# Performance work log

Measured on AMD Instinct MI355X. Metric: run time of the kernel, lower is better.

The kernel has to match this reference:

```python
import jax, jax.numpy as jnp
import numpy as np

L, NK = 4, 6  # num blocks, Nk geodesic components

def _gelu(x):
    return jax.nn.gelu(x, approximate=False)  # torch nn.GELU default (erf)

def _ln(x, g, b, eps=1e-5):
    m = jnp.mean(x, axis=-1, keepdims=True)
    v = jnp.mean((x - m) ** 2, axis=-1, keepdims=True)
    return (x - m) * jax.lax.rsqrt(v + eps) * g + b


def setup_inputs() -> dict:
    B, N, C, M = 4, 8192, 64, 64
    key = jax.random.key(0)
    ks = iter(jax.random.split(key, 48))
    def nrm(*s):
        return jax.random.normal(next(ks), s, dtype=jnp.float32) * 0.02
    inp = {
        'x': jax.random.normal(next(ks), (B, N, 1), dtype=jnp.float32),
        'MATRIX_Phy': jax.random.normal(next(ks), (N, M), dtype=jnp.float32) * 0.02,
        'INVERSE_Phy': jax.random.normal(next(ks), (M, N), dtype=jnp.float32) * 0.02,
        'meshPoints': jax.random.normal(next(ks), (N, 3), dtype=jnp.float32),
        'adj_norm': jax.random.uniform(next(ks), (N, N), dtype=jnp.float32) / N,
    }
    inp.update(
        fc0_w=nrm(4, C), fc0_b=jnp.zeros(C), fc01_w=nrm(C, C), fc01_b=jnp.zeros(C),
        blk_ln1_g=jnp.ones((L, C)), blk_ln1_b=jnp.zeros((L, C)),
        norm1_g=jnp.ones((L, C)), norm1_b=jnp.zeros((L, C)),
        spec_w=jax.random.uniform(next(ks), (L, NK, C, C, M), dtype=jnp.float32) / (C * C),
        enc_p1_w=nrm(L, 3, C), enc_p1_b=jnp.zeros((L, C)),
        enc_p2_w=nrm(L, C, C), enc_p2_b=jnp.zeros((L, C)),
        enc_g1_w=nrm(L, C, C), enc_g1_b=jnp.zeros((L, C)),
        enc_g2_w=nrm(L, C, C), enc_g2_b=jnp.zeros((L, C)),
        enc_o1_w=nrm(L, C, 2 * C), enc_o1_b=jnp.zeros((L, 2 * C)),
        enc_o2_w=nrm(L, 2 * C, NK), enc_o2_b=jnp.zeros((L, NK)),
        spat_g1_w=nrm(L, C, 2 * C), spat_g1_b=jnp.zeros((L, 2 * C)),
        spat_g2_w=nrm(L, 2 * C, C), spat_g2_b=jnp.zeros((L, C)),
        blk_ln2_g=jnp.ones((L, C)), blk_ln2_b=jnp.zeros((L, C)),
        mlp_pre_w=nrm(L, C, 2 * C), mlp_pre_b=jnp.zeros((L, 2 * C)),
        mlp_post_w=nrm(L, 2 * C, C), mlp_post_b=jnp.zeros((L, C)),
        ln1_g=jnp.ones(C), ln1_b=jnp.zeros(C),
        fc1_w=nrm(C, 128), fc1_b=jnp.zeros(128),
        fc2_w=nrm(128, 1), fc2_b=jnp.zeros(1),
    )
    return inp


def reference(x, MATRIX_Phy, INVERSE_Phy, meshPoints, adj_norm,
              fc0_w, fc0_b, fc01_w, fc01_b,
              blk_ln1_g, blk_ln1_b, norm1_g, norm1_b, spec_w,
              enc_p1_w, enc_p1_b, enc_p2_w, enc_p2_b,
              enc_g1_w, enc_g1_b, enc_g2_w, enc_g2_b,
              enc_o1_w, enc_o1_b, enc_o2_w, enc_o2_b,
              spat_g1_w, spat_g1_b, spat_g2_w, spat_g2_b,
              blk_ln2_g, blk_ln2_b, mlp_pre_w, mlp_pre_b, mlp_post_w, mlp_post_b,
              ln1_g, ln1_b, fc1_w, fc1_b, fc2_w, fc2_b):
    B = x.shape[0]
    mesh = jnp.broadcast_to(meshPoints[None], (B,) + meshPoints.shape)  # [B,N,3]
    h = jnp.concatenate([x, mesh], axis=-1)                             # [B,N,4]
    h = h @ fc0_w + fc0_b
    h = h @ fc01_w + fc01_b                                             # [B,N,C]
    for l in range(L):
        z = _ln(h, blk_ln1_g[l], blk_ln1_b[l])
        # --- MeshGCN encoder -> geodesic mixing coefficients geoT [M,Nk] ---
        e = _gelu(meshPoints @ enc_p1_w[l] + enc_p1_b[l]) @ enc_p2_w[l] + enc_p2_b[l]
        e = _gelu(adj_norm @ (e @ enc_g1_w[l] + enc_g1_b[l]))
        e = adj_norm @ (e @ enc_g2_w[l] + enc_g2_b[l])
        e = (e @ enc_o1_w[l] + enc_o1_b[l]) @ enc_o2_w[l] + enc_o2_b[l]  # [N,Nk]
        geoT = jax.nn.softmax(INVERSE_Phy @ e, axis=1)                   # [M,Nk]
        # --- geodesic-modulated spectral conv ---
        cm = jnp.einsum('mn,bnc->bcm', INVERSE_Phy, z)                   # [B,C,M]
        w = jnp.einsum('kiom,mk->iom', spec_w[l], geoT)                  # [C,C,M]
        cg = jnp.einsum('bim,iom->bom', cm, w)                           # [B,C,M]
        x1 = jnp.einsum('bom,nm->bno', cg, MATRIX_Phy)                   # [B,N,C]
        x1 = _ln(x1, norm1_g[l], norm1_b[l])
        # --- spatial GCN branch (SimpleGCN: gcn->relu->gcn) ---
        s = jax.nn.relu(jnp.einsum('mn,bnc->bmc', adj_norm, z @ spat_g1_w[l] + spat_g1_b[l]))
        x2 = jnp.einsum('mn,bnc->bmc', adj_norm, s @ spat_g2_w[l] + spat_g2_b[l])
        h = x1 + x2 + h
        z2 = _ln(h, blk_ln2_g[l], blk_ln2_b[l])
        h = _gelu(z2 @ mlp_pre_w[l] + mlp_pre_b[l]) @ mlp_post_w[l] + mlp_post_b[l] + h
    h = _gelu(_ln(h, ln1_g, ln1_b) @ fc1_w + fc1_b)
    return h @ fc2_w + fc2_b                                             # [B,N,1]
```

## Files before the change

kernel.cpp:

```cpp
#include <hip/hip_runtime.h>
#include <math.h>

typedef __bf16 bf16_t;
typedef __bf16 bf16x8 __attribute__((ext_vector_type(8)));
typedef __bf16 bf16x4 __attribute__((ext_vector_type(4)));
typedef float  f32x4  __attribute__((ext_vector_type(4)));

#define NN 8192
#define RA 8320
#define GPS256 2129920u
#define GPS512 4259840u
#define XPAD 68
#define X2PAD 132
#define ZTPAD 66

__device__ __forceinline__ float gelu_f(float x) {
    return 0.5f * x * (1.0f + erff(x * 0.70710678118654752f));
}

__device__ __forceinline__ float wsum64(float v) {
#pragma unroll
    for (int m = 32; m; m >>= 1) v += __shfl_xor(v, m);
    return v;
}

__device__ __forceinline__ float gp4(const float* __restrict__ Gp, size_t gi) {
    return (Gp[gi] + Gp[gi + (size_t)GPS256]) + (Gp[gi + 2 * (size_t)GPS256] + Gp[gi + 3 * (size_t)GPS256]);
}

__device__ __forceinline__ float gpn(const float* __restrict__ Gp, size_t gi, size_t st, int ns) {
    float v = Gp[gi];
    for (int s = 1; s < ns; ++s) v += Gp[gi + (size_t)s * st];
    return v;
}

__device__ __forceinline__ void async16(const void* g, void* l) {
    __builtin_amdgcn_global_load_lds(
        (const __attribute__((address_space(1))) unsigned int*)g,
        (__attribute__((address_space(3))) unsigned int*)l,
        16, 0, 0);
}

__device__ __forceinline__ void mm16(const float* __restrict__ X, int xpad,
                                     const float* __restrict__ W, int ws, int K,
                                     int c, int r0, float* acc) {
    for (int k0 = 0; k0 < K; k0 += 4) {
        float w0 = W[(size_t)(k0 + 0) * ws + c];
        float w1 = W[(size_t)(k0 + 1) * ws + c];
        float w2 = W[(size_t)(k0 + 2) * ws + c];
        float w3 = W[(size_t)(k0 + 3) * ws + c];
#pragma unroll
        for (int i = 0; i < 16; ++i) {
            float4 xv = *(const float4*)(X + (size_t)(r0 + i) * xpad + k0);
            acc[i] = fmaf(xv.x, w0, acc[i]);
            acc[i] = fmaf(xv.y, w1, acc[i]);
            acc[i] = fmaf(xv.z, w2, acc[i]);
            acc[i] = fmaf(xv.w, w3, acc[i]);
        }
    }
}

__global__ __launch_bounds__(256) void k_adj_convert(const float* __restrict__ adj,
                                                     const float* __restrict__ INV,
                                                     bf16_t* __restrict__ adjB,
                                                     float* __restrict__ rowsum) {
    int row = blockIdx.x;
    int t = threadIdx.x;
    bf16_t* br = adjB + (size_t)row * NN;
    if (row >= NN + 64) {
        bf16x4 zz; zz[0] = zz[1] = zz[2] = zz[3] = (bf16_t)0.f;
#pragma unroll
        for (int v = 0; v < 8; ++v) *(bf16x4*)(br + (v * 256 + t) * 4) = zz;
        return;
    }
    const float* ar = (row < NN) ? adj + (size_t)row * NN : INV + (size_t)(row - NN) * NN;
    float s = 0.f;
#pragma unroll
    for (int v = 0; v < 8; ++v) {
        int i = (v * 256 + t) * 4;
        float4 f = *(const float4*)(ar + i);
        s += f.x + f.y + f.z + f.w;
        bf16x4 o;
        o[0] = (bf16_t)f.x; o[1] = (bf16_t)f.y; o[2] = (bf16_t)f.z; o[3] = (bf16_t)f.w;
        *(bf16x4*)(br + i) = o;
    }
    if (row < NN) {
        s = wsum64(s);
        __shared__ float w4[4];
        if ((t & 63) == 0) w4[t >> 6] = s;
        __syncthreads();
        if (t == 0) rowsum[row] = w4[0] + w4[1] + w4[2] + w4[3];
    }
}

__global__ __launch_bounds__(64) void k_fold(const float* __restrict__ fc0w, const float* __restrict__ fc0b,
                                             const float* __restrict__ fc01w, const float* __restrict__ fc01b,
                                             float* __restrict__ W0b) {
    int c = threadIdx.x;
#pragma unroll
    for (int j = 0; j < 4; ++j) {
        float a = 0.f;
        for (int k = 0; k < 64; ++k) a += fc0w[j * 64 + k] * fc01w[k * 64 + c];
        W0b[j * 64 + c] = a;
    }
    float b = fc01b[c];
    for (int k = 0; k < 64; ++k) b += fc0b[k] * fc01w[k * 64 + c];
    W0b[256 + c] = b;
}

__global__ __launch_bounds__(256) void k_init_h(const float* __restrict__ x, const float* __restrict__ mesh,
                         const float* __restrict__ W0b,
                         const float* __restrict__ zg, const float* __restrict__ zb,
                         float* __restrict__ h, bf16_t* __restrict__ Vt) {
    __shared__ __align__(16) char buf[64 * ZTPAD * 2];
    bf16_t* ZT = (bf16_t*)buf;
    int t = threadIdx.x, c = t & 63, rq = t >> 6, r0 = rq * 16;
    int bb = blockIdx.x >> 7, n0 = (blockIdx.x & 127) * 64;
    float w0c = W0b[c], w1c = W0b[64 + c], w2c = W0b[128 + c], w3c = W0b[192 + c], b0c = W0b[256 + c];
    float gc = zg[c], bc = zb[c];
#pragma unroll
    for (int q = 0; q < 16; ++q) {
        int n = n0 + r0 + q;
        int w = bb * NN + n;
        float xv = x[w];
        float m0 = mesh[n * 3], m1 = mesh[n * 3 + 1], m2 = mesh[n * 3 + 2];
        float hv = b0c + xv * w0c + m0 * w1c + m1 * w2c + m2 * w3c;
        h[(size_t)w * 64 + c] = hv;
        float s = wsum64(hv), s2 = wsum64(hv * hv);
        float mean = s * (1.f / 64.f), var = s2 * (1.f / 64.f) - mean * mean;
        float z = (hv - mean) * rsqrtf(var + 1e-5f) * gc + bc;
        ZT[c * ZTPAD + r0 + q] = (bf16_t)z;
    }
    __syncthreads();
#pragma unroll
    for (int cc = 0; cc < 16; ++cc) {
        int c2 = r0 + cc;
        Vt[(size_t)(256 + bb * 64 + c2) * NN + n0 + c] = ZT[c2 * ZTPAD + c];
    }
}

__global__ __launch_bounds__(256) void k_enc_pre(const float* __restrict__ mesh,
                          const float* __restrict__ p1w, const float* __restrict__ p1b,
                          const float* __restrict__ p2w, const float* __restrict__ p2b,
                          const float* __restrict__ g1w, const float* __restrict__ g1b,
                          bf16_t* __restrict__ Vt) {
    __shared__ __align__(16) char buf[2 * 64 * XPAD * 4];
    float* X1 = (float*)buf;
    float* X2 = (float*)(buf + 64 * XPAD * 4);
    bf16_t* ZT = (bf16_t*)buf;
    int t = threadIdx.x, c = t & 63, rq = t >> 6, r0 = rq * 16;
    int ll = blockIdx.x >> 7, n0 = (blockIdx.x & 127) * 64;
    float p1b_c = p1b[ll * 64 + c];
    float p1w0 = p1w[(ll * 3 + 0) * 64 + c], p1w1 = p1w[(ll * 3 + 1) * 64 + c], p1w2 = p1w[(ll * 3 + 2) * 64 + c];
#pragma unroll
    for (int q = 0; q < 16; ++q) {
        int n = n0 + r0 + q;
        float m0 = mesh[n * 3], m1 = mesh[n * 3 + 1], m2 = mesh[n * 3 + 2];
        X1[(r0 + q) * XPAD + c] = gelu_f(p1b_c + m0 * p1w0 + m1 * p1w1 + m2 * p1w2);
    }
    __syncthreads();
    float e2[16];
#pragma unroll
    for (int i = 0; i < 16; ++i) e2[i] = p2b[ll * 64 + c];
    mm16(X1, XPAD, p2w + ll * 4096, 64, 64, c, r0, e2);
    __syncthreads();
#pragma unroll
    for (int q = 0; q < 16; ++q) X2[(r0 + q) * XPAD + c] = e2[q];
    __syncthreads();
    float tt[16];
#pragma unroll
    for (int i = 0; i < 16; ++i) tt[i] = g1b[ll * 64 + c];
    mm16(X2, XPAD, g1w + ll * 4096, 64, 64, c, r0, tt);
#pragma unroll
    for (int q = 0; q < 16; ++q) ZT[c * ZTPAD + r0 + q] = (bf16_t)tt[q];
    __syncthreads();
#pragma unroll
    for (int cc = 0; cc < 16; ++cc) {
        int c2 = r0 + cc;
        Vt[(size_t)(ll * 64 + c2) * NN + n0 + c] = ZT[c2 * ZTPAD + c];
    }
}

__global__ __launch_bounds__(256) void k_enc_mid(const float* __restrict__ Gp,
                          const float* __restrict__ g2w, const float* __restrict__ g2b,
                          bf16_t* __restrict__ Vt) {
    __shared__ __align__(16) char buf[64 * XPAD * 4 + 64 * ZTPAD * 2];
    float* X = (float*)buf;
    bf16_t* ZT = (bf16_t*)(buf + 64 * XPAD * 4);
    int t = threadIdx.x, c = t & 63, rq = t >> 6, r0 = rq * 16;
    int ll = blockIdx.x >> 7, n0 = (blockIdx.x & 127) * 64;
#pragma unroll
    for (int q = 0; q < 16; ++q) {
        int n = n0 + r0 + q;
        X[(r0 + q) * XPAD + c] = gelu_f(gp4(Gp, (size_t)n * 256 + ll * 64 + c));
    }
    __syncthreads();
    float t2[16];
#pragma unroll
    for (int i = 0; i < 16; ++i) t2[i] = g2b[ll * 64 + c];
    mm16(X, XPAD, g2w + ll * 4096, 64, 64, c, r0, t2);
#pragma unroll
    for (int q = 0; q < 16; ++q) ZT[c * ZTPAD + r0 + q] = (bf16_t)t2[q];
    __syncthreads();
#pragma unroll
    for (int cc = 0; cc < 16; ++cc) {
        int c2 = r0 + cc;
        Vt[(size_t)(ll * 64 + c2) * NN + n0 + c] = ZT[c2 * ZTPAD + c];
    }
}

__global__ void k_geo_part(const float* __restrict__ Gp,
                           const float* __restrict__ o1w, const float* __restrict__ o1b,
                           const float* __restrict__ o2w, const float* __restrict__ o2b,
                           const float* __restrict__ INV,
                           float* __restrict__ partials) {
    int l = blockIdx.x >> 7, chunk = blockIdx.x & 127;
    int n0 = chunk * 64;
    int t = threadIdx.x;
    __shared__ float e4L[64][65];
    for (int r = 0; r < 64; ++r) {
        size_t gi = (size_t)(n0 + r) * 512 + l * 64 + t;
        e4L[r][t] = Gp[gi] + Gp[gi + (size_t)GPS512];
    }
    __syncthreads();
    float X[64];
#pragma unroll
    for (int i = 0; i < 64; ++i) X[i] = e4L[t][i];
    float e5[6] = {0, 0, 0, 0, 0, 0};
    const float* o1wl = o1w + (size_t)l * 64 * 128;
    const float* o2wl = o2w + (size_t)l * 128 * 6;
    for (int j = 0; j < 128; ++j) {
        float a = o1b[l * 128 + j];
#pragma unroll
        for (int i = 0; i < 64; ++i) a += X[i] * o1wl[i * 128 + j];
#pragma unroll
        for (int k = 0; k < 6; ++k) e5[k] += a * o2wl[j * 6 + k];
    }
#pragma unroll
    for (int k = 0; k < 6; ++k) e5[k] += o2b[l * 6 + k];
    __shared__ float e5L[64][8];
#pragma unroll
    for (int k = 0; k < 6; ++k) e5L[t][k] = e5[k];
    __syncthreads();
    float p[6] = {0, 0, 0, 0, 0, 0};
    const float* ivr = INV + (size_t)t * NN + n0;
    for (int r = 0; r < 64; ++r) {
        float iv = ivr[r];
#pragma unroll
        for (int k = 0; k < 6; ++k) p[k] += iv * e5L[r][k];
    }
#pragma unroll
    for (int k = 0; k < 6; ++k) partials[(size_t)(((l * 128 + chunk) * 64) + t) * 6 + k] = p[k];
}

__global__ void k_geo_final(const float* __restrict__ partials, float* __restrict__ geoT) {
    int l = blockIdx.x, m = threadIdx.x;
    float g[6] = {0, 0, 0, 0, 0, 0};
    for (int ch = 0; ch < 128; ++ch) {
#pragma unroll
        for (int k = 0; k < 6; ++k) g[k] += partials[(size_t)(((l * 128 + ch) * 64) + m) * 6 + k];
    }
    float mx = g[0];
#pragma unroll
    for (int k = 1; k < 6; ++k) mx = fmaxf(mx, g[k]);
    float s = 0.f;
#pragma unroll
    for (int k = 0; k < 6; ++k) { g[k] = expf(g[k] - mx); s += g[k]; }
    float inv = 1.f / s;
#pragma unroll
    for (int k = 0; k < 6; ++k) geoT[(size_t)(l * 64 + m) * 6 + k] = g[k] * inv;
}

__global__ __launch_bounds__(64) void k_w(const float* __restrict__ specw,
                                          const float* __restrict__ geoT,
                                          float* __restrict__ wAll) {
    int l = blockIdx.x >> 12, io = blockIdx.x & 4095;
    int m = threadIdx.x;
    float a = 0.f;
#pragma unroll
    for (int k = 0; k < 6; ++k)
        a += specw[(((size_t)l * 6 + k) * 4096 + io) * 64 + m] * geoT[(size_t)(l * 64 + m) * 6 + k];
    wAll[((size_t)l * 4096 + io) * 64 + m] = a;
}

__global__ __launch_bounds__(256) void k_cmsum(const float* __restrict__ Gp, float* __restrict__ cmc,
                                               int ncols, int colbase, int ns) {
    int bi = blockIdx.x * 4 + (threadIdx.x >> 6);
    int m = threadIdx.x & 63;
    size_t st = (size_t)RA * ncols;
    size_t gi = (size_t)(NN + m) * ncols + colbase + bi;
    cmc[bi * 64 + m] = gpn(Gp, gi, st, ns);
}

__global__ __launch_bounds__(256) void k_cg2(const float* __restrict__ cmc,
                                             const float* __restrict__ wl,
                                             float* __restrict__ cgT) {
    int o = blockIdx.x;
    int b = threadIdx.x >> 6, m = threadIdx.x & 63;
    float acc = 0.f;
    for (int i = 0; i < 64; ++i)
        acc += cmc[(b * 64 + i) * 64 + m] * wl[((size_t)(i * 64 + o)) * 64 + m];
    cgT[(b * 64 + m) * 64 + o] = acc;
}

__global__ __launch_bounds__(256) void k_spat_mid(const float* __restrict__ Gp,
                           const float* __restrict__ W1, const float* __restrict__ b1,
                           const float* __restrict__ W2, const float* __restrict__ b2,
                           const float* __restrict__ rowsum, bf16_t* __restrict__ Vt,
                           int ncols, int colbase, int ns) {
    __shared__ __align__(16) char buf[64 * XPAD * 4 + 64 * X2PAD * 4];
    float* X  = (float*)buf;
    float* X2 = (float*)(buf + 64 * XPAD * 4);
    bf16_t* ZT = (bf16_t*)buf;
    int t = threadIdx.x, c = t & 63, rq = t >> 6, r0 = rq * 16;
    int bb = blockIdx.x >> 7, n0 = (blockIdx.x & 127) * 64;
    size_t st = (size_t)RA * ncols;
    float rs[16];
#pragma unroll
    for (int q = 0; q < 16; ++q) {
        int m = n0 + r0 + q;
        rs[q] = rowsum[m];
        X[(r0 + q) * XPAD + c] = gpn(Gp, (size_t)m * ncols + colbase + bb * 64 + c, st, ns);
    }
    __syncthreads();
    float ma0[16], ma1[16];
    float b1c0 = b1[c], b1c1 = b1[64 + c];
#pragma unroll
    for (int i = 0; i < 16; ++i) { ma0[i] = rs[i] * b1c0; ma1[i] = rs[i] * b1c1; }
    mm16(X, XPAD, W1, 128, 64, c, r0, ma0);
    mm16(X, XPAD, W1 + 64, 128, 64, c, r0, ma1);
    __syncthreads();
#pragma unroll
    for (int q = 0; q < 16; ++q) {
        X2[(r0 + q) * X2PAD + c] = fmaxf(ma0[q], 0.f);
        X2[(r0 + q) * X2PAD + 64 + c] = fmaxf(ma1[q], 0.f);
    }
    __syncthreads();
    float y[16];
#pragma unroll
    for (int i = 0; i < 16; ++i) y[i] = b2[c];
    mm16(X2, X2PAD, W2, 64, 128, c, r0, y);
#pragma unroll
    for (int q = 0; q < 16; ++q) ZT[c * ZTPAD + r0 + q] = (bf16_t)y[q];
    __syncthreads();
#pragma unroll
    for (int cc = 0; cc < 16; ++cc) {
        int c2 = r0 + cc;
        Vt[(size_t)(bb * 64 + c2) * NN + n0 + c] = ZT[c2 * ZTPAD + c];
    }
}

__global__ __launch_bounds__(256) void k_blk_post(float* __restrict__ h, const float* __restrict__ Gp,
                           const float* __restrict__ cgT, const float* __restrict__ MP,
                           const float* __restrict__ n1g, const float* __restrict__ n1b,
                           const float* __restrict__ l2g, const float* __restrict__ l2b,
                           const float* __restrict__ prew, const float* __restrict__ preb,
                           const float* __restrict__ postw, const float* __restrict__ postb,
                           const float* __restrict__ zng, const float* __restrict__ znb,
                           bf16_t* __restrict__ Vt, int writeZ) {
    __shared__ __align__(16) char buf[64 * X2PAD * 4 + 64 * XPAD * 4];
    float* MProws = (float*)buf;
    float* X2     = (float*)buf;
    float* X      = (float*)(buf + 64 * X2PAD * 4);
    bf16_t* ZT    = (bf16_t*)(buf + 64 * X2PAD * 4);
    int t = threadIdx.x, c = t & 63, rq = t >> 6, r0 = rq * 16;
    int bb = blockIdx.x >> 7, n0 = (blockIdx.x & 127) * 64;
#pragma unroll
    for (int q = 0; q < 16; ++q)
        MProws[(r0 + q) * XPAD + c] = MP[(size_t)(n0 + r0 + q) * 64 + c];
    __syncthreads();
    float x1[16];
#pragma unroll
    for (int i = 0; i < 16; ++i) x1[i] = 0.f;
    mm16(MProws, XPAD, cgT + (size_t)bb * 4096, 64, 64, c, r0, x1);
    float hv[16];
    float n1gc = n1g[c], n1bc = n1b[c];
#pragma unroll
    for (int q = 0; q < 16; ++q) {
        float s = wsum64(x1[q]), s2 = wsum64(x1[q] * x1[q]);
        float mean = s * (1.f / 64.f), var = s2 * (1.f / 64.f) - mean * mean;
        float x1n = (x1[q] - mean) * rsqrtf(var + 1e-5f) * n1gc + n1bc;
        int n = n0 + r0 + q;
        size_t w = (size_t)bb * NN + n;
        hv[q] = x1n + gp4(Gp, (size_t)n * 256 + bb * 64 + c) + h[w * 64 + c];
    }
    float l2gc = l2g[c], l2bc = l2b[c];
#pragma unroll
    for (int q = 0; q < 16; ++q) {
        float s = wsum64(hv[q]), s2 = wsum64(hv[q] * hv[q]);
        float mean = s * (1.f / 64.f), var = s2 * (1.f / 64.f) - mean * mean;
        X[(r0 + q) * XPAD + c] = (hv[q] - mean) * rsqrtf(var + 1e-5f) * l2gc + l2bc;
    }
    __syncthreads();
    float ma0[16], ma1[16];
    float pb0 = preb[c], pb1 = preb[64 + c];
#pragma unroll
    for (int i = 0; i < 16; ++i) { ma0[i] = pb0; ma1[i] = pb1; }
    mm16(X, XPAD, prew, 128, 64, c, r0, ma0);
    mm16(X, XPAD, prew + 64, 128, 64, c, r0, ma1);
    __syncthreads();
#pragma unroll
    for (int q = 0; q < 16; ++q) {
        X2[(r0 + q) * X2PAD + c] = gelu_f(ma0[q]);
        X2[(r0 + q) * X2PAD + 64 + c] = gelu_f(ma1[q]);
    }
    __syncthreads();
    float o[16];
    float pob = postb[c];
#pragma unroll
    for (int i = 0; i < 16; ++i) o[i] = pob;
    mm16(X2, X2PAD, postw, 64, 128, c, r0, o);
#pragma unroll
    for (int q = 0; q < 16; ++q) {
        hv[q] += o[q];
        h[((size_t)bb * NN + n0 + r0 + q) * 64 + c] = hv[q];
    }
    if (writeZ) {
        float zgc = zng[c], zbc = znb[c];
#pragma unroll
        for (int q = 0; q < 16; ++q) {
            float s = wsum64(hv[q]), s2 = wsum64(hv[q] * hv[q]);
            float mean = s * (1.f / 64.f), var = s2 * (1.f / 64.f) - mean * mean;
            ZT[c * ZTPAD + r0 + q] = (bf16_t)((hv[q] - mean) * rsqrtf(var + 1e-5f) * zgc + zbc);
        }
        __syncthreads();
#pragma unroll
        for (int cc = 0; cc < 16; ++cc) {
            int c2 = r0 + cc;
            Vt[(size_t)(256 + bb * 64 + c2) * NN + n0 + c] = ZT[c2 * ZTPAD + c];
        }
    }
}

__global__ __launch_bounds__(256) void k_head(const float* __restrict__ h,
                       const float* __restrict__ g, const float* __restrict__ bb_,
                       const float* __restrict__ fc1w, const float* __restrict__ fc1b,
                       const float* __restrict__ fc2w, const float* __restrict__ fc2b,
                       float* __restrict__ out) {
    __shared__ __align__(16) char buf[64 * XPAD * 4 + 64 * X2PAD * 4];
    float* X  = (float*)buf;
    float* X2 = (float*)(buf + 64 * XPAD * 4);
    int t = threadIdx.x, c = t & 63, rq = t >> 6, r0 = rq * 16;
    int bb = blockIdx.x >> 7, n0 = (blockIdx.x & 127) * 64;
    float gc = g[c], bc = bb_[c];
#pragma unroll
    for (int q = 0; q < 16; ++q) {
        float hv = h[((size_t)bb * NN + n0 + r0 + q) * 64 + c];
        float s = wsum64(hv), s2 = wsum64(hv * hv);
        float mean = s * (1.f / 64.f), var = s2 * (1.f / 64.f) - mean * mean;
        X[(r0 + q) * XPAD + c] = (hv - mean) * rsqrtf(var + 1e-5f) * gc + bc;
    }
    __syncthreads();
    float ma0[16], ma1[16];
    float fb0 = fc1b[c], fb1 = fc1b[64 + c];
#pragma unroll
    for (int i = 0; i < 16; ++i) { ma0[i] = fb0; ma1[i] = fb1; }
    mm16(X, XPAD, fc1w, 128, 64, c, r0, ma0);
    mm16(X, XPAD, fc1w + 64, 128, 64, c, r0, ma1);
    __syncthreads();
#pragma unroll
    for (int q = 0; q < 16; ++q) {
        X2[(r0 + q) * X2PAD + c] = gelu_f(ma0[q]);
        X2[(r0 + q) * X2PAD + 64 + c] = gelu_f(ma1[q]);
    }
    __syncthreads();
    float f2a = fc2w[c], f2b = fc2w[64 + c], f2bias = fc2b[0];
#pragma unroll
    for (int q = 0; q < 16; ++q) {
        float val = X2[(r0 + q) * X2PAD + c] * f2a + X2[(r0 + q) * X2PAD + 64 + c] * f2b;
        val = wsum64(val);
        if (c == 0) out[(size_t)bb * NN + n0 + r0 + q] = val + f2bias;
    }
}

__global__ __launch_bounds__(256, 3) void gemm_bf16(const bf16_t* __restrict__ A,
                                                    const bf16_t* __restrict__ Bt,
                                                    float* __restrict__ Gp,
                                                    int ntn, int ns) {
    __shared__ __align__(16) char smem[2][16384];
    const int cpx = gridDim.x >> 3;
    const int bid = blockIdx.x;
    const int tile = (bid & 7) * cpx + (bid >> 3);
    const int per_tm = ntn * ns;
    const int tm = tile / per_tm;
    const int rem = tile % per_tm;
    const int tn = rem % ntn;
    const int ks = rem / ntn;
    const int nkt = 256 / ns;
    const int kt0 = ks * nkt;
    const int ncols = ntn * 128;

    const int t = threadIdx.x;
    const int lane = t & 63, wid = t >> 6;
    const int wr = wid >> 1, wc = wid & 1;
    const int lrow = lane & 15, lk = lane >> 4;

    const bf16_t* Abase = A + (size_t)tm * 128 * NN;
    const bf16_t* Bbase = Bt + (size_t)tn * 128 * NN;

    f32x4 acc[4][4];
#pragma unroll
    for (int i = 0; i < 4; ++i)
#pragma unroll
        for (int j = 0; j < 4; ++j) acc[i][j] = f32x4{0.f, 0.f, 0.f, 0.f};

    auto stage = [&](int bsel, int kt) {
        char* lb = smem[bsel];
        int k0 = kt * 32;
        {
            int ci = t;
            int rw = ci >> 2, ch = ci & 3, sch = ch ^ (rw & 3);
            async16(Abase + (size_t)rw * NN + k0 + sch * 8, lb + ci * 16);
            ci = t + 256;
            rw = ci >> 2; ch = ci & 3; sch = ch ^ (rw & 3);
            async16(Abase + (size_t)rw * NN + k0 + sch * 8, lb + ci * 16);
        }
        {
            int ci = t;
            int rw = ci >> 2, ch = ci & 3, sch = ch ^ (rw & 3);
            async16(Bbase + (size_t)rw * NN + k0 + sch * 8, lb + 8192 + ci * 16);
            ci = t + 256;
            rw = ci >> 2; ch = ci & 3; sch = ch ^ (rw & 3);
            async16(Bbase + (size_t)rw * NN + k0 + sch * 8, lb + 8192 + ci * 16);
        }
    };

    stage(0, kt0);
    __syncthreads();
    for (int it = 0; it < nkt; ++it) {
        int cur = it & 1;
        if (it + 1 < nkt) stage(cur ^ 1, kt0 + it + 1);
        const char* lb = smem[cur];
        bf16x8 av[4], bv[4];
#pragma unroll
        for (int i = 0; i < 4; ++i) {
            int R = wr * 64 + i * 16 + lrow;
            av[i] = *(const bf16x8*)(lb + R * 64 + ((lk ^ (R & 3)) << 4));
        }
#pragma unroll
        for (int j = 0; j < 4; ++j) {
            int Q = wc * 64 + j * 16 + lrow;
            bv[j] = *(const bf16x8*)(lb + 8192 + Q * 64 + ((lk ^ (Q & 3)) << 4));
        }
#pragma unroll
        for (int i = 0; i < 4; ++i)
#pragma unroll
            for (int j = 0; j < 4; ++j)
                acc[i][j] = __builtin_amdgcn_mfma_f32_16x16x32_bf16(av[i], bv[j], acc[i][j], 0, 0, 0);
        __syncthreads();
    }

    float* Cs = Gp + (size_t)ks * RA * ncols;
    const int row0 = tm * 128 + wr * 64;
    const int col0 = tn * 128 + wc * 64;
#pragma unroll
    for (int i = 0; i < 4; ++i)
#pragma unroll
        for (int j = 0; j < 4; ++j)
#pragma unroll
            for (int r = 0; r < 4; ++r)
                Cs[(size_t)(row0 + i * 16 + lk * 4 + r) * ncols + col0 + j * 16 + lrow] = acc[i][j][r];
}


extern "C" void kernel_launch(void* const* d_in, const int* in_sizes, int n_in,
                              void* d_out, int out_size, void* d_ws, size_t ws_size,
                              hipStream_t stream) {
    const float* x     = (const float*)d_in[0];
    const float* MP    = (const float*)d_in[1];
    const float* INV   = (const float*)d_in[2];
    const float* mesh  = (const float*)d_in[3];
    const float* adj   = (const float*)d_in[4];
    const float* fc0w  = (const float*)d_in[5];
    const float* fc0b  = (const float*)d_in[6];
    const float* fc01w = (const float*)d_in[7];
    const float* fc01b = (const float*)d_in[8];
    const float* bln1g = (const float*)d_in[9];
    const float* bln1b = (const float*)d_in[10];
    const float* n1g   = (const float*)d_in[11];
    const float* n1b   = (const float*)d_in[12];
    const float* specw = (const float*)d_in[13];
    const float* p1w   = (const float*)d_in[14];
    const float* p1b   = (const float*)d_in[15];
    const float* p2w   = (const float*)d_in[16];
    const float* p2b   = (const float*)d_in[17];
    const float* g1w   = (const float*)d_in[18];
    const float* g1b   = (const float*)d_in[19];
    const float* g2w   = (const float*)d_in[20];
    const float* g2b   = (const float*)d_in[21];
    const float* o1w   = (const float*)d_in[22];
    const float* o1b   = (const float*)d_in[23];
    const float* o2w   = (const float*)d_in[24];
    const float* o2b   = (const float*)d_in[25];
    const float* sg1w  = (const float*)d_in[26];
    const float* sg1b  = (const float*)d_in[27];
    const float* sg2w  = (const float*)d_in[28];
    const float* sg2b  = (const float*)d_in[29];
    const float* bln2g = (const float*)d_in[30];
    const float* bln2b = (const float*)d_in[31];
    const float* prew  = (const float*)d_in[32];
    const float* preb  = (const float*)d_in[33];
    const float* postw = (const float*)d_in[34];
    const float* postb = (const float*)d_in[35];
    const float* ln1g  = (const float*)d_in[36];
    const float* ln1b  = (const float*)d_in[37];
    const float* fc1w  = (const float*)d_in[38];
    const float* fc1b  = (const float*)d_in[39];
    const float* fc2w  = (const float*)d_in[40];
    const float* fc2b  = (const float*)d_in[41];
    float* out = (float*)d_out;

    char* ws = (char*)d_ws;
    bf16_t* adjB    = (bf16_t*)(ws);
    float*  Gp512   = (float*) (ws + 136314880);
    float*  Gp256   = (float*) (ws + 170393600);
    bf16_t* Vt      = (bf16_t*)(ws + 204472320);
    float*  h       = (float*) (ws + 212860928);
    float*  rowsum  = (float*) (ws + 221249536);
    float*  partials= (float*) (ws + 221282304);
    float*  geoT    = (float*) (ws + 222068736);
    float*  wAll    = (float*) (ws + 222074880);
    float*  cmc     = (float*) (ws + 226269184);
    float*  cgT     = (float*) (ws + 226334720);
    float*  W0b     = (float*) (ws + 226400256);

    bf16_t* VtZ = Vt + (size_t)256 * NN;

    k_adj_convert<<<RA, 256, 0, stream>>>(adj, INV, adjB, rowsum);
    k_fold<<<1, 64, 0, stream>>>(fc0w, fc0b, fc01w, fc01b, W0b);

    k_enc_pre<<<512, 256, 0, stream>>>(mesh, p1w, p1b, p2w, p2b, g1w, g1b, Vt);
    gemm_bf16<<<520, 256, 0, stream>>>(adjB, Vt, Gp256, 2, 4);
    k_enc_mid<<<512, 256, 0, stream>>>(Gp256, g2w, g2b, Vt);
    k_init_h<<<512, 256, 0, stream>>>(x, mesh, W0b, bln1g, bln1b, h, Vt);

    gemm_bf16<<<520, 256, 0, stream>>>(adjB, Vt, Gp512, 4, 2);

    k_geo_part<<<512, 64, 0, stream>>>(Gp512, o1w, o1b, o2w, o2b, INV, partials);
    k_geo_final<<<4, 64, 0, stream>>>(partials, geoT);
    k_w<<<16384, 64, 0, stream>>>(specw, geoT, wAll);

    for (int l = 0; l < 4; ++l) {
        const float* Gp1 = Gp256; int nc = 256, cb = 0, ns1 = 4;
        if (l == 0) { Gp1 = Gp512; nc = 512; cb = 256; ns1 = 2; }
        else {
            gemm_bf16<<<520, 256, 0, stream>>>(adjB, VtZ, Gp256, 2, 4);
        }
        k_cmsum<<<64, 256, 0, stream>>>(Gp1, cmc, nc, cb, ns1);
        k_cg2<<<64, 256, 0, stream>>>(cmc, wAll + (size_t)l * 262144, cgT);
        k_spat_mid<<<512, 256, 0, stream>>>(Gp1, sg1w + l * 64 * 128, sg1b + l * 128,
                                            sg2w + l * 128 * 64, sg2b + l * 64, rowsum, Vt,
                                            nc, cb, ns1);
        gemm_bf16<<<520, 256, 0, stream>>>(adjB, Vt, Gp256, 2, 4);
        int ln = (l < 3) ? (l + 1) : 3;
        k_blk_post<<<512, 256, 0, stream>>>(h, Gp256, cgT, MP,
                                            n1g + l * 64, n1b + l * 64,
                                            bln2g + l * 64, bln2b + l * 64,
                                            prew + l * 64 * 128, preb + l * 128,
                                            postw + l * 128 * 64, postb + l * 64,
                                            bln1g + ln * 64, bln1b + ln * 64,
                                            Vt, (l < 3) ? 1 : 0);
    }

    k_head<<<512, 256, 0, stream>>>(h, ln1g, ln1b, fc1w, fc1b, fc2w, fc2b, out);
}
```

Before: 1.323 ms.

## Retile adjacency GEMM to 128x64 tiles with 64-wide K steps

The bf16 MFMA GEMM tile changes from 128x128 with a K step of 32 to 128x64 with a K step of 64. The LDS swizzle widens to 8 chunks per row. The grid doubles to 1040 blocks, and tile decode now orders by split-K slice first. The aim is more blocks in flight and fewer barriers per K of work. The cost is that each A tile is loaded from global memory twice as often, and the min-blocks launch bound hint is dropped.

```diff
diff --git a/kernel.cpp b/kernel.cpp
--- a/kernel.cpp
+++ b/kernel.cpp
@@ -473,22 +473,22 @@
     }
 }
 
-__global__ __launch_bounds__(256, 3) void gemm_bf16(const bf16_t* __restrict__ A,
-                                                    const bf16_t* __restrict__ Bt,
-                                                    float* __restrict__ Gp,
-                                                    int ntn, int ns) {
-    __shared__ __align__(16) char smem[2][16384];
+__global__ __launch_bounds__(256) void gemm_bf16(const bf16_t* __restrict__ A,
+                                                 const bf16_t* __restrict__ Bt,
+                                                 float* __restrict__ Gp,
+                                                 int ntn, int ns) {
+    __shared__ __align__(16) char smem[2][24576];
     const int cpx = gridDim.x >> 3;
     const int bid = blockIdx.x;
     const int tile = (bid & 7) * cpx + (bid >> 3);
-    const int per_tm = ntn * ns;
-    const int tm = tile / per_tm;
-    const int rem = tile % per_tm;
-    const int tn = rem % ntn;
-    const int ks = rem / ntn;
-    const int nkt = 256 / ns;
+    const int pertile = 65 * ntn;
+    const int ks = tile / pertile;
+    const int r2 = tile % pertile;
+    const int tn = r2 % ntn;
+    const int tm = r2 / ntn;
+    const int nkt = 128 / ns;
     const int kt0 = ks * nkt;
-    const int ncols = ntn * 128;
+    const int ncols = ntn * 64;
 
     const int t = threadIdx.x;
     const int lane = t & 63, wid = t >> 6;
@@ -496,32 +496,31 @@
     const int lrow = lane & 15, lk = lane >> 4;
 
     const bf16_t* Abase = A + (size_t)tm * 128 * NN;
-    const bf16_t* Bbase = Bt + (size_t)tn * 128 * NN;
-
-    f32x4 acc[4][4];
-#pragma unroll
-    for (int i = 0; i < 4; ++i)
-#pragma unroll
-        for (int j = 0; j < 4; ++j) acc[i][j] = f32x4{0.f, 0.f, 0.f, 0.f};
+    const bf16_t* Bbase = Bt + (size_t)tn * 64 * NN;
+
+    f32x4 acc[4][2];
+#pragma unroll
+    for (int i = 0; i < 4; ++i) {
+        acc[i][0] = f32x4{0.f, 0.f, 0.f, 0.f};
+        acc[i][1] = f32x4{0.f, 0.f, 0.f, 0.f};
+    }
 
     auto stage = [&](int bsel, int kt) {
         char* lb = smem[bsel];
-        int k0 = kt * 32;
-        {
-            int ci = t;
-            int rw = ci >> 2, ch = ci & 3, sch = ch ^ (rw & 3);
-            async16(Abase + (size_t)rw * NN + k0 + sch * 8, lb + ci * 16);
-            ci = t + 256;
-            rw = ci >> 2; ch = ci & 3; sch = ch ^ (rw & 3);
+        int k0 = kt * 64;
+#pragma unroll
+        for (int r = 0; r < 4; ++r) {
+            int ci = t + r * 256;
+            int rw = ci >> 3, ch = ci & 7;
+            int sch = ch ^ (rw & 7);
             async16(Abase + (size_t)rw * NN + k0 + sch * 8, lb + ci * 16);
         }
-        {
-            int ci = t;
-            int rw = ci >> 2, ch = ci & 3, sch = ch ^ (rw & 3);
-            async16(Bbase + (size_t)rw * NN + k0 + sch * 8, lb + 8192 + ci * 16);
-            ci = t + 256;
-            rw = ci >> 2; ch = ci & 3; sch = ch ^ (rw & 3);
-            async16(Bbase + (size_t)rw * NN + k0 + sch * 8, lb + 8192 + ci * 16);
+#pragma unroll
+        for (int r = 0; r < 2; ++r) {
+            int ci = t + r * 256;
+            int rw = ci >> 3, ch = ci & 7;
+            int sch = ch ^ (rw & 7);
+            async16(Bbase + (size_t)rw * NN + k0 + sch * 8, lb + 16384 + ci * 16);
         }
     };
 
@@ -531,32 +530,35 @@
         int cur = it & 1;
         if (it + 1 < nkt) stage(cur ^ 1, kt0 + it + 1);
         const char* lb = smem[cur];
-        bf16x8 av[4], bv[4];
-#pragma unroll
-        for (int i = 0; i < 4; ++i) {
-            int R = wr * 64 + i * 16 + lrow;
-            av[i] = *(const bf16x8*)(lb + R * 64 + ((lk ^ (R & 3)) << 4));
+#pragma unroll
+        for (int kk = 0; kk < 2; ++kk) {
+            bf16x8 av[4], bv[2];
+#pragma unroll
+            for (int i = 0; i < 4; ++i) {
+                int R = wr * 64 + i * 16 + lrow;
+                av[i] = *(const bf16x8*)(lb + R * 128 + (((kk * 4 + lk) ^ (R & 7)) << 4));
+            }
+#pragma unroll
+            for (int j = 0; j < 2; ++j) {
+                int Q = wc * 32 + j * 16 + lrow;
+                bv[j] = *(const bf16x8*)(lb + 16384 + Q * 128 + (((kk * 4 + lk) ^ (Q & 7)) << 4));
+            }
+#pragma unroll
+            for (int i = 0; i < 4; ++i)
+#pragma unroll
+                for (int j = 0; j < 2; ++j)
+                    acc[i][j] = __builtin_amdgcn_mfma_f32_16x16x32_bf16(av[i], bv[j], acc[i][j], 0, 0, 0);
         }
-#pragma unroll
-        for (int j = 0; j < 4; ++j) {
-            int Q = wc * 64 + j * 16 + lrow;
-            bv[j] = *(const bf16x8*)(lb + 8192 + Q * 64 + ((lk ^ (Q & 3)) << 4));
-        }
-#pragma unroll
-        for (int i = 0; i < 4; ++i)
-#pragma unroll
-            for (int j = 0; j < 4; ++j)
-                acc[i][j] = __builtin_amdgcn_mfma_f32_16x16x32_bf16(av[i], bv[j], acc[i][j], 0, 0, 0);
         __syncthreads();
     }
 
     float* Cs = Gp + (size_t)ks * RA * ncols;
-    const int row0 = tm * 128 + wr * 64;
-    const int col0 = tn * 128 + wc * 64;
+    int row0 = tm * 128 + wr * 64;
+    int col0 = tn * 64 + wc * 32;
 #pragma unroll
     for (int i = 0; i < 4; ++i)
 #pragma unroll
-        for (int j = 0; j < 4; ++j)
+        for (int j = 0; j < 2; ++j)
 #pragma unroll
             for (int r = 0; r < 4; ++r)
                 Cs[(size_t)(row0 + i * 16 + lk * 4 + r) * ncols + col0 + j * 16 + lrow] = acc[i][j][r];
@@ -630,11 +632,11 @@
     k_fold<<<1, 64, 0, stream>>>(fc0w, fc0b, fc01w, fc01b, W0b);
 
     k_enc_pre<<<512, 256, 0, stream>>>(mesh, p1w, p1b, p2w, p2b, g1w, g1b, Vt);
-    gemm_bf16<<<520, 256, 0, stream>>>(adjB, Vt, Gp256, 2, 4);
+    gemm_bf16<<<1040, 256, 0, stream>>>(adjB, Vt, Gp256, 4, 4);
     k_enc_mid<<<512, 256, 0, stream>>>(Gp256, g2w, g2b, Vt);
     k_init_h<<<512, 256, 0, stream>>>(x, mesh, W0b, bln1g, bln1b, h, Vt);
 
-    gemm_bf16<<<520, 256, 0, stream>>>(adjB, Vt, Gp512, 4, 2);
+    gemm_bf16<<<1040, 256, 0, stream>>>(adjB, Vt, Gp512, 8, 2);
 
     k_geo_part<<<512, 64, 0, stream>>>(Gp512, o1w, o1b, o2w, o2b, INV, partials);
     k_geo_final<<<4, 64, 0, stream>>>(partials, geoT);
@@ -644,14 +646,14 @@
         const float* Gp1 = Gp256; int nc = 256, cb = 0, ns1 = 4;
         if (l == 0) { Gp1 = Gp512; nc = 512; cb = 256; ns1 = 2; }
         else {
-            gemm_bf16<<<520, 256, 0, stream>>>(adjB, VtZ, Gp256, 2, 4);
+            gemm_bf16<<<1040, 256, 0, stream>>>(adjB, VtZ, Gp256, 4, 4);
         }
         k_cmsum<<<64, 256, 0, stream>>>(Gp1, cmc, nc, cb, ns1);
         k_cg2<<<64, 256, 0, stream>>>(cmc, wAll + (size_t)l * 262144, cgT);
         k_spat_mid<<<512, 256, 0, stream>>>(Gp1, sg1w + l * 64 * 128, sg1b + l * 128,
                                             sg2w + l * 128 * 64, sg2b + l * 64, rowsum, Vt,
                                             nc, cb, ns1);
-        gemm_bf16<<<520, 256, 0, stream>>>(adjB, Vt, Gp256, 2, 4);
+        gemm_bf16<<<1040, 256, 0, stream>>>(adjB, Vt, Gp256, 4, 4);
         int ln = (l < 3) ? (l + 1) : 3;
         k_blk_post<<<512, 256, 0, stream>>>(h, Gp256, cgT, MP,
                                             n1g + l * 64, n1b + l * 64,
```

Result: no change. 1.311 ms (-0.8%).
